# Optimization experiments

Measured on AMD Instinct MI355X. Metric: run time of the kernel, lower is better.

Reference implementation:

```python
import jax, jax.numpy as jnp
import numpy as np

N_HITS = 49152
HIT_F = 256
INST_F = 32
N_IT_CONST = 1024
Q_MIN = 0.5   # ObjCondensationLoss default q_min
S_B = 1.0     # ObjCondensationLoss default background strength


def setup_inputs() -> dict:
    key = jax.random.key(0)
    ks = jax.random.split(key, 6)
    x = jax.random.normal(ks[0], (N_HITS, HIT_F), jnp.float32)
    W_beta = jax.random.normal(ks[1], (HIT_F, 1), jnp.float32) / np.sqrt(HIT_F).astype(np.float32)
    b_beta = jnp.zeros((1,), jnp.float32)
    W_coord = jax.random.normal(ks[2], (HIT_F, INST_F), jnp.float32) / np.sqrt(HIT_F).astype(np.float32)
    b_coord = jnp.zeros((INST_F,), jnp.float32)
    temp = jnp.zeros((), jnp.float32)  # nn.Parameter(torch.tensor(0.0))
    # true instance labels per hit; pin first N_IT hits so every instance is populated
    y_i = jax.random.randint(ks[3], (N_HITS,), 0, N_IT_CONST)
    y_i = y_i.at[:N_IT_CONST].set(jnp.arange(N_IT_CONST))
    idx = jnp.arange(N_HITS)
    noise = (idx % 5 == 0) & (idx >= N_IT_CONST)
    y_i = jnp.where(noise, -1, y_i).astype(jnp.int64)
    y_semantic = jax.random.randint(ks[4], (N_HITS,), 0, 7).astype(jnp.int32)
    # hit -> true-instance membership edges (E_H_IT), fixed shape built eagerly
    yv = np.asarray(y_i)
    e0 = np.nonzero(yv >= 0)[0]
    edge_index = jnp.asarray(np.stack([e0, yv[e0]]), dtype=jnp.int32)
    return {"x": x, "W_beta": W_beta, "b_beta": b_beta, "W_coord": W_coord,
            "b_coord": b_coord, "temp": temp, "y_i": y_i,
            "y_semantic": y_semantic, "edge_index": edge_index, "n_it": N_IT_CONST}


def _obj_condensation_loss(ox, beta, y_i, edge_index, n_it):
    """Object condensation loss -> stack([background_loss, potential_loss])."""
    n = ox.shape[0]
    beta_c = jnp.clip(beta, 1e-4, 1.0 - 1e-4)
    q = jnp.arctanh(beta_c) ** 2 + Q_MIN  # charge per hit, [N]
    e_h, e_i = edge_index[0], edge_index[1]
    qe = q[e_h]
    # condensation point alpha_k = member hit with max charge (segment argmax)
    seg_max = jax.ops.segment_max(qe, e_i, num_segments=n_it)
    is_max = qe >= seg_max[e_i]
    alpha = jax.ops.segment_min(jnp.where(is_max, e_h, n), e_i, num_segments=n_it)
    alpha = jnp.clip(alpha, 0, n - 1)
    x_a = ox[alpha]        # [K, D]
    q_a = q[alpha]         # [K]
    beta_a = beta_c[alpha]  # [K]
    # attractive potential over membership edges: q_i * q_alpha * ||x_i - x_alpha||^2
    d2_att = jnp.sum((ox[e_h] - x_a[e_i]) ** 2, axis=-1)
    v_att = jnp.sum(qe * q_a[e_i] * d2_att)
    # repulsive potential over all (hit, instance) non-member pairs: hinge(1 - dist)
    d2 = (jnp.sum(ox * ox, axis=1)[:, None] + jnp.sum(x_a * x_a, axis=1)[None, :]
          - 2.0 * ox @ x_a.T)  # [N, K]
    dist = jnp.sqrt(jnp.maximum(d2, 0.0) + 1e-12)
    hinge = jnp.maximum(1.0 - dist, 0.0)
    member = jnp.zeros((n, n_it), jnp.float32).at[e_h, e_i].set(1.0)
    v_rep = jnp.sum((q[:, None] * q_a[None, :]) * hinge * (1.0 - member))
    l_v = (v_att + v_rep) / n
    # background loss: push beta_alpha -> 1, noise-hit beta -> 0
    noise = y_i < 0
    n_noise = jnp.maximum(jnp.sum(noise), 1)
    l_b = jnp.mean(1.0 - beta_a) + S_B * jnp.sum(jnp.where(noise, beta_c, 0.0)) / n_noise
    return jnp.stack([l_b, l_v])


def reference(x, W_beta, b_beta, W_coord, b_coord, temp, y_i, y_semantic, edge_index, n_it):
    beta = jax.nn.sigmoid(x @ W_beta + b_beta)[:, 0]  # h.of, [N]
    ox = x @ W_coord + b_coord                        # h.ox, [N, D]
    loss_vec = _obj_condensation_loss(ox, beta, y_i, edge_index, n_it)
    loss_vec = loss_vec * jnp.exp(-temp)  # temperature-weighted (b, v)
    return loss_vec.sum() + temp          # train-stage scalar loss
```

## Files before the change

### kernel.cpp

```cpp
#include <hip/hip_runtime.h>
#include <math.h>

#define NH 49152
#define KI 1024
#define DD 32
#define HF 256

#define WS_PART  0
#define WS_SEG64 8
#define WS_WT    2056
#define WS_A12   (WS_WT + 8448)
#define WS_H12   (WS_A12 + 12*KI)
#define WS_XA    (WS_H12 + 12*NH)
#define WS_OX    (WS_XA + KI*DD)

__global__ __launch_bounds__(256) void k_prep(const float* __restrict__ Wc,
                                              const float* __restrict__ Wb,
                                              float* __restrict__ ws) {
    const int i = blockIdx.x * 256 + threadIdx.x;
    if (i < 8192) {
        const int w = i >> 11, r = i & 2047;
        const int win = r >> 5, kj = r & 31;
        const int kk = kj >> 3, j = kj & 7;
        ws[WS_WT + i] = Wc[(size_t)(win * 4 + kk) * 32 + w * 8 + j];
    } else if (i < 8448) {
        ws[WS_WT + i] = Wb[i - 8192];
    }
    if (i < 512) *(float4*)(ws + WS_SEG64 + (size_t)i * 4) = make_float4(0.f, 0.f, 0.f, 0.f);
    if (i < 8) ws[WS_PART + i] = 0.0f;
}

__global__ __launch_bounds__(256, 3) void k_gemm(
        const float* __restrict__ x, const float* __restrict__ bb,
        const float* __restrict__ bcrd, const int* __restrict__ yi,
        float* __restrict__ ws) {
    const int t = threadIdx.x;
    const int w = __builtin_amdgcn_readfirstlane(t >> 6);
    const int l = t & 63;
    const int h = blockIdx.x * 64 + l;
    const float* __restrict__ wt3 = ws + WS_WT + w * 2048;
    const float* __restrict__ wtb = ws + WS_WT + 8192;
    const float* __restrict__ xp  = x + (size_t)h * HF;

    float acc[8];
    #pragma unroll
    for (int j = 0; j < 8; ++j) acc[j] = 0.0f;
    float accb = 0.0f;

#define COMPUTE(XV, WIN) { \
        const float* wp = wt3 + (WIN) * 32; \
        _Pragma("unroll") \
        for (int j = 0; j < 8; ++j) { \
            acc[j] = fmaf(XV.x, wp[j],      acc[j]); \
            acc[j] = fmaf(XV.y, wp[8 + j],  acc[j]); \
            acc[j] = fmaf(XV.z, wp[16 + j], acc[j]); \
            acc[j] = fmaf(XV.w, wp[24 + j], acc[j]); \
        } \
        if (w == 3) { \
            const float* wpb = wtb + (WIN) * 4; \
            accb = fmaf(XV.x, wpb[0], accb); \
            accb = fmaf(XV.y, wpb[1], accb); \
            accb = fmaf(XV.z, wpb[2], accb); \
            accb = fmaf(XV.w, wpb[3], accb); \
        } \
    }

    float4 x0 = *(const float4*)(xp + 0);
    float4 x1 = *(const float4*)(xp + 4);
    float4 x2 = *(const float4*)(xp + 8);
    float4 x3 = *(const float4*)(xp + 12);
    for (int S4 = 0; S4 < 15; ++S4) {
        const int wb4 = S4 * 4;
        COMPUTE(x0, wb4 + 0);  x0 = *(const float4*)(xp + wb4 * 4 + 16);
        COMPUTE(x1, wb4 + 1);  x1 = *(const float4*)(xp + wb4 * 4 + 20);
        COMPUTE(x2, wb4 + 2);  x2 = *(const float4*)(xp + wb4 * 4 + 24);
        COMPUTE(x3, wb4 + 3);  x3 = *(const float4*)(xp + wb4 * 4 + 28);
    }
    COMPUTE(x0, 60);
    COMPUTE(x1, 61);
    COMPUTE(x2, 62);
    COMPUTE(x3, 63);

    const float4 ba0 = *(const float4*)(bcrd + w * 8);
    const float4 ba1 = *(const float4*)(bcrd + w * 8 + 4);
    const float4 o0 = {acc[0] + ba0.x, acc[1] + ba0.y, acc[2] + ba0.z, acc[3] + ba0.w};
    const float4 o1 = {acc[4] + ba1.x, acc[5] + ba1.y, acc[6] + ba1.z, acc[7] + ba1.w};
    *(float4*)(ws + WS_OX + (size_t)h * DD + w * 8)     = o0;
    *(float4*)(ws + WS_OX + (size_t)h * DD + w * 8 + 4) = o1;

    if (w == 0) {
        const float s8 = o0.x*o0.x + o0.y*o0.y + o0.z*o0.z + o0.w*o0.w
                       + o1.x*o1.x + o1.y*o1.y + o1.z*o1.z + o1.w*o1.w;
        float* hr = ws + WS_H12 + (size_t)h * 12;
        *(float4*)(hr)     = o0;
        *(float4*)(hr + 4) = o1;
        hr[8] = 0.5f * s8;
    }
    if (w == 3) {
        const float z    = accb + bb[0];
        const float beta = 1.0f / (1.0f + expf(-z));
        const float bcv  = fminf(fmaxf(beta, 1e-4f), 0.9999f);
        const float at   = atanhf(bcv);
        float* hr = ws + WS_H12 + (size_t)h * 12;
        hr[9]  = at * at + 0.5f;
        hr[10] = bcv;
        const int y = yi[h];
        float    nb  = (y < 0) ? bcv : 0.0f;
        unsigned cnt = (y < 0) ? 1u : 0u;
        for (int off = 32; off > 0; off >>= 1) {
            nb  += __shfl_down(nb, off);
            cnt += __shfl_down(cnt, off);
        }
        if (l == 0) {
            atomicAdd(ws + WS_PART + 2, nb);
            atomicAdd((unsigned int*)(ws + WS_PART + 3), cnt);
        }
    }
}

__global__ __launch_bounds__(256) void k_segmax(const int* __restrict__ eh, const int* __restrict__ ei,
                                                int E, const float* __restrict__ h12,
                                                unsigned long long* __restrict__ seg) {
    int e = blockIdx.x * 256 + threadIdx.x;
    if (e < E) {
        int h = eh[e];
        float q = h12[(size_t)h * 12 + 9];
        unsigned long long pk = ((unsigned long long)__float_as_uint(q) << 32)
                              | (unsigned)(NH - 1 - h);
        atomicMax(seg + ei[e], pk);
    }
}

__global__ __launch_bounds__(256) void k_gather(float* __restrict__ ws) {
    const int k = blockIdx.x * 256 + threadIdx.x;
    unsigned long long pk = ((const unsigned long long*)(ws + WS_SEG64))[k];
    int a = NH - 1 - (int)(unsigned)(pk & 0xffffffffu);
    a = max(0, min(a, NH - 1));
    float4 v0, v1;
    float s8 = 0.0f;
    #pragma unroll
    for (int d0 = 0; d0 < DD; d0 += 4) {
        float4 v = *(const float4*)(ws + WS_OX + (size_t)a * DD + d0);
        *(float4*)(ws + WS_XA + (size_t)k * DD + d0) = v;
        if (d0 == 0) { v0 = v; s8 += v.x*v.x + v.y*v.y + v.z*v.z + v.w*v.w; }
        if (d0 == 4) { v1 = v; s8 += v.x*v.x + v.y*v.y + v.z*v.z + v.w*v.w; }
    }
    *(float4*)(ws + WS_A12 + (size_t)k * 12)     = v0;
    *(float4*)(ws + WS_A12 + (size_t)k * 12 + 4) = v1;
    ws[WS_A12 + (size_t)k * 12 + 8] = 0.5f * (s8 - 1.0f);
    ws[WS_A12 + (size_t)k * 12 + 9] = ws[WS_H12 + (size_t)a * 12 + 9];
    float omba = 1.0f - ws[WS_H12 + (size_t)a * 12 + 10];
    for (int off = 32; off > 0; off >>= 1) omba += __shfl_down(omba, off);
    if ((threadIdx.x & 63) == 0) atomicAdd(ws + WS_PART + 4, omba);
}

__global__ __launch_bounds__(256) void k_att(const int* __restrict__ eh, const int* __restrict__ ei,
                                             int E, float* __restrict__ ws) {
    const int t = threadIdx.x;
    const int e = blockIdx.x * 256 + t;
    float c = 0.0f;
    if (e < E) {
        const int h = eh[e], k = ei[e];
        const float* a = ws + WS_OX + (size_t)h * DD;
        const float* b = ws + WS_XA + (size_t)k * DD;
        float d2 = 0.0f;
        #pragma unroll
        for (int d0 = 0; d0 < DD; d0 += 4) {
            float4 av = *(const float4*)(a + d0);
            float4 bv = *(const float4*)(b + d0);
            float dx = av.x - bv.x; d2 = fmaf(dx, dx, d2);
            float dy = av.y - bv.y; d2 = fmaf(dy, dy, d2);
            float dz = av.z - bv.z; d2 = fmaf(dz, dz, d2);
            float dw = av.w - bv.w; d2 = fmaf(dw, dw, d2);
        }
        c = ws[WS_H12 + (size_t)h * 12 + 9] * ws[WS_A12 + (size_t)k * 12 + 9] * d2;
    }
    for (int off = 32; off > 0; off >>= 1) c += __shfl_down(c, off);
    __shared__ float red[4];
    if ((t & 63) == 0) red[t >> 6] = c;
    __syncthreads();
    if (t == 0) atomicAdd(ws + WS_PART + 1, red[0] + red[1] + red[2] + red[3]);
}

__global__ __launch_bounds__(256, 4) void k_rep(const int* __restrict__ yi,
        const float* __restrict__ a12, const float* __restrict__ h12,
        const float* __restrict__ ox, const float* __restrict__ xa,
        float* __restrict__ part) {
    __shared__ float al[128 * 12];
    const int t  = threadIdx.x;
    const int bh = blockIdx.x % 96;
    const int bk = blockIdx.x / 96;
    const int k0 = bk * 128;

    for (int i = t; i < 128 * 12; i += 256)
        al[i] = a12[(size_t)k0 * 12 + i];
    __syncthreads();

    const int h1 = bh * 512 + t;
    const int h2 = h1 + 256;
    const float4 p0  = *(const float4*)(h12 + (size_t)h1 * 12);
    const float4 p1  = *(const float4*)(h12 + (size_t)h1 * 12 + 4);
    const float2 cq1 = *(const float2*)(h12 + (size_t)h1 * 12 + 8);
    const float4 s0  = *(const float4*)(h12 + (size_t)h2 * 12);
    const float4 s1  = *(const float4*)(h12 + (size_t)h2 * 12 + 4);
    const float2 cq2 = *(const float2*)(h12 + (size_t)h2 * 12 + 8);
    const int yh1 = yi[h1], yh2 = yi[h2];
    float loc = 0.0f;

    #pragma unroll 4
    for (int r = 0; r < 128; ++r) {
        const float4 b0  = *(const float4*)(al + r * 12);
        const float4 b1  = *(const float4*)(al + r * 12 + 4);
        const float2 bcq = *(const float2*)(al + r * 12 + 8);
        float acc1 = -cq1.x - bcq.x;
        acc1 = fmaf(p0.x, b0.x, acc1);
        acc1 = fmaf(p0.y, b0.y, acc1);
        acc1 = fmaf(p0.z, b0.z, acc1);
        acc1 = fmaf(p0.w, b0.w, acc1);
        acc1 = fmaf(p1.x, b1.x, acc1);
        acc1 = fmaf(p1.y, b1.y, acc1);
        acc1 = fmaf(p1.z, b1.z, acc1);
        acc1 = fmaf(p1.w, b1.w, acc1);
        float acc2 = -cq2.x - bcq.x;
        acc2 = fmaf(s0.x, b0.x, acc2);
        acc2 = fmaf(s0.y, b0.y, acc2);
        acc2 = fmaf(s0.z, b0.z, acc2);
        acc2 = fmaf(s0.w, b0.w, acc2);
        acc2 = fmaf(s1.x, b1.x, acc2);
        acc2 = fmaf(s1.y, b1.y, acc2);
        acc2 = fmaf(s1.z, b1.z, acc2);
        acc2 = fmaf(s1.w, b1.w, acc2);
        if (acc1 > 0.0f) {
            const int kg = k0 + r;
            if (yh1 != kg) {
                float d2 = 1.0f - 2.0f * acc1;
                const float* hp  = ox + (size_t)h1 * DD;
                const float* apf = xa + (size_t)kg * DD;
                #pragma unroll
                for (int d = 8; d < DD; d += 4) {
                    float4 av = *(const float4*)(hp + d);
                    float4 bv = *(const float4*)(apf + d);
                    float dx = av.x - bv.x; d2 = fmaf(dx, dx, d2);
                    float dy = av.y - bv.y; d2 = fmaf(dy, dy, d2);
                    float dz = av.z - bv.z; d2 = fmaf(dz, dz, d2);
                    float dw = av.w - bv.w; d2 = fmaf(dw, dw, d2);
                }
                float dist = sqrtf(fmaxf(d2, 0.0f) + 1e-12f);
                float hin  = 1.0f - dist;
                if (hin > 0.0f) loc += cq1.y * bcq.y * hin;
            }
        }
        if (acc2 > 0.0f) {
            const int kg = k0 + r;
            if (yh2 != kg) {
                float d2 = 1.0f - 2.0f * acc2;
                const float* hp  = ox + (size_t)h2 * DD;
                const float* apf = xa + (size_t)kg * DD;
                #pragma unroll
                for (int d = 8; d < DD; d += 4) {
                    float4 av = *(const float4*)(hp + d);
                    float4 bv = *(const float4*)(apf + d);
                    float dx = av.x - bv.x; d2 = fmaf(dx, dx, d2);
                    float dy = av.y - bv.y; d2 = fmaf(dy, dy, d2);
                    float dz = av.z - bv.z; d2 = fmaf(dz, dz, d2);
                    float dw = av.w - bv.w; d2 = fmaf(dw, dw, d2);
                }
                float dist = sqrtf(fmaxf(d2, 0.0f) + 1e-12f);
                float hin  = 1.0f - dist;
                if (hin > 0.0f) loc += cq2.y * bcq.y * hin;
            }
        }
    }
    for (int off = 32; off > 0; off >>= 1) loc += __shfl_down(loc, off);
    __shared__ float red[4];
    if ((t & 63) == 0) red[t >> 6] = loc;
    __syncthreads();
    if (t == 0) atomicAdd(part + 0, red[0] + red[1] + red[2] + red[3]);
}

__global__ void k_final(const float* __restrict__ temp, float* __restrict__ ws,
                        float* __restrict__ out) {
    float vrep  = ws[WS_PART + 0];
    float vatt  = ws[WS_PART + 1];
    float nsum  = ws[WS_PART + 2];
    unsigned nn = *(const unsigned int*)(ws + WS_PART + 3);
    float somba = ws[WS_PART + 4];
    float lb = somba * (1.0f / (float)KI) + nsum / (float)(nn < 1u ? 1u : nn);
    float lv = (vatt + vrep) / (float)NH;
    float tv = temp[0];
    out[0] = (lb + lv) * expf(-tv) + tv;
}

extern "C" void kernel_launch(void* const* d_in, const int* in_sizes, int n_in,
                              void* d_out, int out_size, void* d_ws, size_t ws_size,
                              hipStream_t stream) {
    const float* x    = (const float*)d_in[0];
    const float* Wb   = (const float*)d_in[1];
    const float* bb   = (const float*)d_in[2];
    const float* Wc   = (const float*)d_in[3];
    const float* bcrd = (const float*)d_in[4];
    const float* temp = (const float*)d_in[5];
    const int*   yi   = (const int*)d_in[6];
    const int*   ep   = (const int*)d_in[8];
    const int E = in_sizes[8] / 2;
    const int* eh = ep;
    const int* ei = ep + E;
    float* ws  = (float*)d_ws;
    float* out = (float*)d_out;

    k_prep<<<34, 256, 0, stream>>>(Wc, Wb, ws);
    k_gemm<<<NH / 64, 256, 0, stream>>>(x, bb, bcrd, yi, ws);
    const int eb = (E + 255) / 256;
    k_segmax<<<eb, 256, 0, stream>>>(eh, ei, E, ws + WS_H12,
                                     (unsigned long long*)(ws + WS_SEG64));
    k_gather<<<KI / 256, 256, 0, stream>>>(ws);
    k_att<<<eb, 256, 0, stream>>>(eh, ei, E, ws);
    k_rep<<<96 * 8, 256, 0, stream>>>(yi, ws + WS_A12, ws + WS_H12,
                                      ws + WS_OX, ws + WS_XA, ws);
    k_final<<<1, 1, 0, stream>>>(temp, ws, out);
}
```

Baseline: 108.1 us.

## Stage x rows via LDS async loads with register-held weights; merge att/rep kernels

The GEMM kernel now keeps each lane's slice of the coordinate weights in registers and broadcasts them with readlane. x tiles are streamed into double-buffered shared memory using global_load_lds, replacing per-thread strided float4 loads from global memory. The weight permutation in k_prep is changed to match the new layout. The attractive-edge and repulsive kernels are also fused into one launch, with the block index choosing the role, to save a launch and overlap the two. Risks include higher register pressure, barrier overhead in the staged loop, and mixing heterogeneous blocks in one grid.

```diff
diff --git a/kernel.cpp b/kernel.cpp
--- a/kernel.cpp
+++ b/kernel.cpp
@@ -5,6 +5,7 @@
 #define KI 1024
 #define DD 32
 #define HF 256
+#define REPB 768
 
 #define WS_PART  0
 #define WS_SEG64 8
@@ -14,17 +15,28 @@
 #define WS_XA    (WS_H12 + 12*NH)
 #define WS_OX    (WS_XA + KI*DD)
 
+typedef __attribute__((address_space(1))) const unsigned int gu32;
+typedef __attribute__((address_space(3))) unsigned int lu32;
+
+__device__ __forceinline__ float rl(float v, int lane) {
+    return __uint_as_float(__builtin_amdgcn_readlane(__float_as_uint(v), lane));
+}
+
 __global__ __launch_bounds__(256) void k_prep(const float* __restrict__ Wc,
                                               const float* __restrict__ Wb,
                                               float* __restrict__ ws) {
     const int i = blockIdx.x * 256 + threadIdx.x;
     if (i < 8192) {
-        const int w = i >> 11, r = i & 2047;
-        const int win = r >> 5, kj = r & 31;
-        const int kk = kj >> 3, j = kj & 7;
-        ws[WS_WT + i] = Wc[(size_t)(win * 4 + kk) * 32 + w * 8 + j];
+        const int w = i >> 11, r2 = i & 2047;
+        const int l = r2 >> 5, q = r2 & 31;
+        const int dk = q >> 3, col = q & 7;
+        const int k = (l >> 3) * 32 + (l & 7) * 4 + dk;
+        ws[WS_WT + i] = Wc[(size_t)k * 32 + w * 8 + col];
     } else if (i < 8448) {
-        ws[WS_WT + i] = Wb[i - 8192];
+        const int r2 = i - 8192;
+        const int l = r2 >> 2, dk = r2 & 3;
+        const int k = (l >> 3) * 32 + (l & 7) * 4 + dk;
+        ws[WS_WT + i] = Wb[k];
     }
     if (i < 512) *(float4*)(ws + WS_SEG64 + (size_t)i * 4) = make_float4(0.f, 0.f, 0.f, 0.f);
     if (i < 8) ws[WS_PART + i] = 0.0f;
@@ -34,52 +46,67 @@
         const float* __restrict__ x, const float* __restrict__ bb,
         const float* __restrict__ bcrd, const int* __restrict__ yi,
         float* __restrict__ ws) {
-    const int t = threadIdx.x;
-    const int w = __builtin_amdgcn_readfirstlane(t >> 6);
-    const int l = t & 63;
-    const int h = blockIdx.x * 64 + l;
-    const float* __restrict__ wt3 = ws + WS_WT + w * 2048;
-    const float* __restrict__ wtb = ws + WS_WT + 8192;
-    const float* __restrict__ xp  = x + (size_t)h * HF;
+    __shared__ float xs[2][8][256];
+    const int t0 = threadIdx.x;
+    const int w  = __builtin_amdgcn_readfirstlane(t0 >> 6);
+    const int l  = t0 & 63;
+    const int h  = blockIdx.x * 64 + l;
+    const float* __restrict__ wbase = ws + WS_WT + w * 2048;
+    const float* __restrict__ xrow  = x + (size_t)h * HF;
+
+    float wr[32];
+    #pragma unroll
+    for (int q = 0; q < 8; ++q) {
+        const float4 v = *(const float4*)(wbase + l * 32 + q * 4);
+        wr[q * 4 + 0] = v.x; wr[q * 4 + 1] = v.y;
+        wr[q * 4 + 2] = v.z; wr[q * 4 + 3] = v.w;
+    }
+    float br[4] = {0.f, 0.f, 0.f, 0.f};
+    if (w == 3) {
+        const float4 v = *(const float4*)(ws + WS_WT + 8192 + l * 4);
+        br[0] = v.x; br[1] = v.y; br[2] = v.z; br[3] = v.w;
+    }
 
     float acc[8];
     #pragma unroll
     for (int j = 0; j < 8; ++j) acc[j] = 0.0f;
     float accb = 0.0f;
 
-#define COMPUTE(XV, WIN) { \
-        const float* wp = wt3 + (WIN) * 32; \
-        _Pragma("unroll") \
-        for (int j = 0; j < 8; ++j) { \
-            acc[j] = fmaf(XV.x, wp[j],      acc[j]); \
-            acc[j] = fmaf(XV.y, wp[8 + j],  acc[j]); \
-            acc[j] = fmaf(XV.z, wp[16 + j], acc[j]); \
-            acc[j] = fmaf(XV.w, wp[24 + j], acc[j]); \
-        } \
-        if (w == 3) { \
-            const float* wpb = wtb + (WIN) * 4; \
-            accb = fmaf(XV.x, wpb[0], accb); \
-            accb = fmaf(XV.y, wpb[1], accb); \
-            accb = fmaf(XV.z, wpb[2], accb); \
-            accb = fmaf(XV.w, wpb[3], accb); \
-        } \
-    }
-
-    float4 x0 = *(const float4*)(xp + 0);
-    float4 x1 = *(const float4*)(xp + 4);
-    float4 x2 = *(const float4*)(xp + 8);
-    float4 x3 = *(const float4*)(xp + 12);
-    for (int S4 = 0; S4 < 15; ++S4) {
-        const int wb4 = S4 * 4;
-        COMPUTE(x0, wb4 + 0);  x0 = *(const float4*)(xp + wb4 * 4 + 16);
-        COMPUTE(x1, wb4 + 1);  x1 = *(const float4*)(xp + wb4 * 4 + 20);
-        COMPUTE(x2, wb4 + 2);  x2 = *(const float4*)(xp + wb4 * 4 + 24);
-        COMPUTE(x3, wb4 + 3);  x3 = *(const float4*)(xp + wb4 * 4 + 28);
-    }
-    COMPUTE(x0, 60);
-    COMPUTE(x1, 61);
-    COMPUTE(x2, 62);
-    COMPUTE(x3, 63);
+#define STAGE(buf, c1) { \
+    const float* s0 = xrow + (c1) * 32 + (2 * w) * 4; \
+    __builtin_amdgcn_global_load_lds((gu32*)(const void*)s0, \
+        (lu32*)(void*)&xs[buf][2 * w][0], 16, 0, 0); \
+    const float* s1 = s0 + 4; \
+    __builtin_amdgcn_global_load_lds((gu32*)(const void*)s1, \
+        (lu32*)(void*)&xs[buf][2 * w + 1][0], 16, 0, 0); }
+
+#define DK(dk, xc) { \
+    acc[0] = fmaf(xc, rl(wr[(dk)*8 + 0], ls), acc[0]); \
+    acc[1] = fmaf(xc, rl(wr[(dk)*8 + 1], ls), acc[1]); \
+    acc[2] = fmaf(xc, rl(wr[(dk)*8 + 2], ls), acc[2]); \
+    acc[3] = fmaf(xc, rl(wr[(dk)*8 + 3], ls), acc[3]); \
+    acc[4] = fmaf(xc, rl(wr[(dk)*8 + 4], ls), acc[4]); \
+    acc[5] = fmaf(xc, rl(wr[(dk)*8 + 5], ls), acc[5]); \
+    acc[6] = fmaf(xc, rl(wr[(dk)*8 + 6], ls), acc[6]); \
+    acc[7] = fmaf(xc, rl(wr[(dk)*8 + 7], ls), acc[7]); \
+    if (w == 3) accb = fmaf(xc, rl(br[dk], ls), accb); }
+
+    STAGE(0, 0);
+    __syncthreads();
+    for (int c = 0; c < 8; ++c) {
+        if (c < 7) STAGE((c + 1) & 1, c + 1);
+        const int lb = c * 8;
+        #pragma unroll
+        for (int t = 0; t < 8; ++t) {
+            const float4 xv = *(const float4*)&xs[c & 1][t][l * 4];
+            const int ls = lb + t;
+            DK(0, xv.x)
+            DK(1, xv.y)
+            DK(2, xv.z)
+            DK(3, xv.w)
+        }
+        __syncthreads();
+    }
 
     const float4 ba0 = *(const float4*)(bcrd + w * 8);
     const float4 ba1 = *(const float4*)(bcrd + w * 8 + 4);
@@ -154,44 +181,46 @@
     if ((threadIdx.x & 63) == 0) atomicAdd(ws + WS_PART + 4, omba);
 }
 
-__global__ __launch_bounds__(256) void k_att(const int* __restrict__ eh, const int* __restrict__ ei,
-                                             int E, float* __restrict__ ws) {
+__global__ __launch_bounds__(256, 4) void k_attrep(
+        const int* __restrict__ eh, const int* __restrict__ ei, int E,
+        const int* __restrict__ yi, float* __restrict__ ws) {
+    __shared__ float al[128 * 12];
+    __shared__ float red[4];
+    const float* __restrict__ a12 = ws + WS_A12;
+    const float* __restrict__ h12 = ws + WS_H12;
+    const float* __restrict__ ox  = ws + WS_OX;
+    const float* __restrict__ xa  = ws + WS_XA;
     const int t = threadIdx.x;
-    const int e = blockIdx.x * 256 + t;
-    float c = 0.0f;
-    if (e < E) {
-        const int h = eh[e], k = ei[e];
-        const float* a = ws + WS_OX + (size_t)h * DD;
-        const float* b = ws + WS_XA + (size_t)k * DD;
-        float d2 = 0.0f;
-        #pragma unroll
-        for (int d0 = 0; d0 < DD; d0 += 4) {
-            float4 av = *(const float4*)(a + d0);
-            float4 bv = *(const float4*)(b + d0);
-            float dx = av.x - bv.x; d2 = fmaf(dx, dx, d2);
-            float dy = av.y - bv.y; d2 = fmaf(dy, dy, d2);
-            float dz = av.z - bv.z; d2 = fmaf(dz, dz, d2);
-            float dw = av.w - bv.w; d2 = fmaf(dw, dw, d2);
-        }
-        c = ws[WS_H12 + (size_t)h * 12 + 9] * ws[WS_A12 + (size_t)k * 12 + 9] * d2;
-    }
-    for (int off = 32; off > 0; off >>= 1) c += __shfl_down(c, off);
-    __shared__ float red[4];
-    if ((t & 63) == 0) red[t >> 6] = c;
-    __syncthreads();
-    if (t == 0) atomicAdd(ws + WS_PART + 1, red[0] + red[1] + red[2] + red[3]);
-}
-
-__global__ __launch_bounds__(256, 4) void k_rep(const int* __restrict__ yi,
-        const float* __restrict__ a12, const float* __restrict__ h12,
-        const float* __restrict__ ox, const float* __restrict__ xa,
-        float* __restrict__ part) {
-    __shared__ float al[128 * 12];
-    const int t  = threadIdx.x;
+
+    if (blockIdx.x >= REPB) {
+        const int e = (blockIdx.x - REPB) * 256 + t;
+        float cv = 0.0f;
+        if (e < E) {
+            const int h = eh[e], k = ei[e];
+            const float* a = ox + (size_t)h * DD;
+            const float* b = xa + (size_t)k * DD;
+            float d2 = 0.0f;
+            #pragma unroll
+            for (int d0 = 0; d0 < DD; d0 += 4) {
+                float4 av = *(const float4*)(a + d0);
+                float4 bv = *(const float4*)(b + d0);
+                float dx = av.x - bv.x; d2 = fmaf(dx, dx, d2);
+                float dy = av.y - bv.y; d2 = fmaf(dy, dy, d2);
+                float dz = av.z - bv.z; d2 = fmaf(dz, dz, d2);
+                float dw = av.w - bv.w; d2 = fmaf(dw, dw, d2);
+            }
+            cv = h12[(size_t)h * 12 + 9] * a12[(size_t)k * 12 + 9] * d2;
+        }
+        for (int off = 32; off > 0; off >>= 1) cv += __shfl_down(cv, off);
+        if ((t & 63) == 0) red[t >> 6] = cv;
+        __syncthreads();
+        if (t == 0) atomicAdd(ws + WS_PART + 1, red[0] + red[1] + red[2] + red[3]);
+        return;
+    }
+
     const int bh = blockIdx.x % 96;
     const int bk = blockIdx.x / 96;
     const int k0 = bk * 128;
-
     for (int i = t; i < 128 * 12; i += 256)
         al[i] = a12[(size_t)k0 * 12 + i];
     __syncthreads();
@@ -272,10 +301,9 @@
         }
     }
     for (int off = 32; off > 0; off >>= 1) loc += __shfl_down(loc, off);
-    __shared__ float red[4];
     if ((t & 63) == 0) red[t >> 6] = loc;
     __syncthreads();
-    if (t == 0) atomicAdd(part + 0, red[0] + red[1] + red[2] + red[3]);
+    if (t == 0) atomicAdd(ws + WS_PART + 0, red[0] + red[1] + red[2] + red[3]);
 }
 
 __global__ void k_final(const float* __restrict__ temp, float* __restrict__ ws,
@@ -308,14 +336,12 @@
     float* ws  = (float*)d_ws;
     float* out = (float*)d_out;
 
-    k_prep<<<34, 256, 0, stream>>>(Wc, Wb, ws);
+    k_prep<<<33, 256, 0, stream>>>(Wc, Wb, ws);
     k_gemm<<<NH / 64, 256, 0, stream>>>(x, bb, bcrd, yi, ws);
     const int eb = (E + 255) / 256;
     k_segmax<<<eb, 256, 0, stream>>>(eh, ei, E, ws + WS_H12,
                                      (unsigned long long*)(ws + WS_SEG64));
     k_gather<<<KI / 256, 256, 0, stream>>>(ws);
-    k_att<<<eb, 256, 0, stream>>>(eh, ei, E, ws);
-    k_rep<<<96 * 8, 256, 0, stream>>>(yi, ws + WS_A12, ws + WS_H12,
-                                      ws + WS_OX, ws + WS_XA, ws);
+    k_attrep<<<REPB + eb, 256, 0, stream>>>(eh, ei, E, yi, ws);
     k_final<<<1, 1, 0, stream>>>(temp, ws, out);
 }
```

Result: slower. 117.3 us (+8.5%).
